# Kernel optimization log

Measured on AMD Instinct MI355X. Metric: run time of the kernel, lower is better.

## Reference

```python
import jax, jax.numpy as jnp
import numpy as np

B, S, E, H = 4, 2048, 512, 8
D = E // H


def setup_inputs() -> dict:
    key = jax.random.key(0)
    ks = jax.random.split(key, 12)
    sc = 0.02
    return {
        "x": jax.random.normal(ks[0], (B, S, E), jnp.float32),
        "edge_bias": jax.random.normal(ks[1], (B, S, S), jnp.float32),
        "attn_mask": jax.random.randint(ks[2], (B, 1, S, S), 0, 2, jnp.int32),
        "Wq": jax.random.normal(ks[3], (E, E), jnp.float32) * sc,
        "bq": jnp.zeros((E,), jnp.float32),
        "Wk": jax.random.normal(ks[4], (E, E), jnp.float32) * sc,
        "bk": jnp.zeros((E,), jnp.float32),
        "Wv": jax.random.normal(ks[5], (E, E), jnp.float32) * sc,
        "bv": jnp.zeros((E,), jnp.float32),
        "Wo": jax.random.normal(ks[6], (E, E), jnp.float32) * sc,
        "bo": jnp.zeros((E,), jnp.float32),
    }


def reference(x, edge_bias, attn_mask, Wq, bq, Wk, bk, Wv, bv, Wo, bo):
    scale = D ** -0.5
    # projections -> [B, H, S, D]
    def proj(W, b):
        return (x @ W.T + b).reshape(B, S, H, D).transpose(0, 2, 1, 3)
    q = proj(Wq, bq)
    k = proj(Wk, bk)
    v = proj(Wv, bv)
    # scores [B, H, S, S] with edge bias and mask before softmax
    scores = jnp.einsum("bhqd,bhkd->bhqk", q, k) * scale
    scores = scores + edge_bias[:, None, :, :]
    scores = jnp.where(attn_mask == 0, -jnp.inf, scores)
    probs = jax.nn.softmax(scores, axis=-1)
    out = jnp.einsum("bhqk,bhkd->bhqd", probs, v)
    out = out.transpose(0, 2, 1, 3).reshape(B, S, E)
    return out @ Wo.T + bo
```

## Files before the change

kernel.cpp:

```cpp
#include <hip/hip_runtime.h>
#include <hip/hip_bf16.h>
#include <stdint.h>

#define DEV static __device__ __forceinline__

typedef float f32x4 __attribute__((ext_vector_type(4)));
typedef int   i32x4 __attribute__((ext_vector_type(4)));
typedef unsigned short u16x4 __attribute__((ext_vector_type(4)));
typedef __bf16 bf16x8 __attribute__((ext_vector_type(8)));

constexpr int Bb = 4, Ss = 2048, Ee = 512, Hh = 8, Dd = 64;
constexpr float LOG2E = 1.4426950408889634f;

DEV unsigned short f2bf(float f) {
  unsigned u = __float_as_uint(f);
  u += 0x7fff + ((u >> 16) & 1);
  return (unsigned short)(u >> 16);
}
DEV float bf2f(unsigned short h) { return __uint_as_float(((unsigned)h) << 16); }

DEV void gload16(const void* g, void* l) {
  __builtin_amdgcn_global_load_lds((__attribute__((address_space(1))) void*)(g),
                                   (__attribute__((address_space(3))) void*)(l), 16, 0, 0);
}

__global__ void k_cvt(const float* __restrict__ src, unsigned short* __restrict__ dst, int n4) {
  int i = blockIdx.x * 256 + threadIdx.x;
  if (i >= n4) return;
  f32x4 v = *(const f32x4*)(src + (size_t)i * 4);
  u16x4 o;
#pragma unroll
  for (int j = 0; j < 4; ++j) o[j] = f2bf(v[j]);
  *(u16x4*)(dst + (size_t)i * 4) = o;
}

__global__ void k_mb(const float* __restrict__ bias, const int* __restrict__ mask,
                     unsigned short* __restrict__ mb, int n4) {
  int i = blockIdx.x * 256 + threadIdx.x;
  if (i >= n4) return;
  f32x4 v = *(const f32x4*)(bias + (size_t)i * 4);
  i32x4 m = *(const i32x4*)(mask + (size_t)i * 4);
  u16x4 o;
  const unsigned short NEG = f2bf(-1e38f * LOG2E);
#pragma unroll
  for (int j = 0; j < 4; ++j) o[j] = m[j] ? f2bf(v[j] * LOG2E) : NEG;
  *(u16x4*)(mb + (size_t)i * 4) = o;
}

template <int MODE>
__global__ __launch_bounds__(256) void k_gemm(
    const unsigned short* __restrict__ A, const unsigned short* __restrict__ Bw,
    const float* __restrict__ b0, const float* __restrict__ b1, const float* __restrict__ b2,
    unsigned short* __restrict__ oq, unsigned short* __restrict__ ok,
    unsigned short* __restrict__ ovt, float* __restrict__ of32) {
  __shared__ unsigned short Asl[128 * 32];
  __shared__ unsigned short Bsl[128 * 32];
  const int tid = threadIdx.x;
  const int wave = tid >> 6, lane = tid & 63;
  const int l15 = lane & 15, lg = lane >> 4;
  const int brow = blockIdx.x, bcol = blockIdx.y;
  const int wm = (wave >> 1) * 64, wn = (wave & 1) * 64;

  f32x4 acc[4][4] = {};

  for (int k0 = 0; k0 < 512; k0 += 32) {
    __syncthreads();
#pragma unroll
    for (int rnd = 0; rnd < 2; ++rnd) {
      int vid = rnd * 256 + tid;
      int r = vid >> 2, c = vid & 3;
      gload16(A + (size_t)(brow * 128 + r) * 512 + k0 + c * 8,
              Asl + (size_t)(rnd * 256 + wave * 64) * 8);
      gload16(Bw + (size_t)(bcol * 128 + r) * 512 + k0 + c * 8,
              Bsl + (size_t)(rnd * 256 + wave * 64) * 8);
    }
    __syncthreads();
    bf16x8 af[4], bfr[4];
#pragma unroll
    for (int m = 0; m < 4; ++m) af[m] = *(const bf16x8*)(Asl + (wm + m * 16 + l15) * 32 + lg * 8);
#pragma unroll
    for (int n = 0; n < 4; ++n) bfr[n] = *(const bf16x8*)(Bsl + (wn + n * 16 + l15) * 32 + lg * 8);
#pragma unroll
    for (int m = 0; m < 4; ++m)
#pragma unroll
      for (int n = 0; n < 4; ++n)
        acc[m][n] = __builtin_amdgcn_mfma_f32_16x16x32_bf16(af[m], bfr[n], acc[m][n], 0, 0, 0);
  }

  if (MODE == 0) {
    const int Nbase = bcol * 128;
    const int mat = Nbase >> 9;
    const int colb = Nbase & 511;
    const float* bp = (mat == 0) ? b0 : ((mat == 1) ? b1 : b2);
#pragma unroll
    for (int m = 0; m < 4; ++m)
#pragma unroll
      for (int n = 0; n < 4; ++n) {
        const int col = colb + wn + n * 16 + l15;
        const int h = col >> 6, d = col & 63;
        const float bv = bp[col];
#pragma unroll
        for (int j = 0; j < 4; ++j) {
          const int M = brow * 128 + wm + m * 16 + lg * 4 + j;
          const int b = M >> 11, s = M & 2047;
          float outv = acc[m][n][j] + bv;
          if (mat == 0) outv *= 0.125f * LOG2E;
          const unsigned short hv = f2bf(outv);
          if (mat == 0)
            oq[(((size_t)(b * Hh + h)) * Ss + s) * Dd + d] = hv;
          else if (mat == 1)
            ok[(((size_t)(b * Hh + h)) * Ss + s) * Dd + d] = hv;
          else
            ovt[(((size_t)(b * Hh + h)) * Dd + d) * Ss + s] = hv;
        }
      }
  } else {
#pragma unroll
    for (int m = 0; m < 4; ++m)
#pragma unroll
      for (int n = 0; n < 4; ++n) {
        const int col = bcol * 128 + wn + n * 16 + l15;
        const float bv = b0[col];
#pragma unroll
        for (int j = 0; j < 4; ++j) {
          const int M = brow * 128 + wm + m * 16 + lg * 4 + j;
          of32[(size_t)M * 512 + col] = acc[m][n][j] + bv;
        }
      }
  }
}

__global__ __launch_bounds__(256, 4) void k_attn(
    const unsigned short* __restrict__ q, const unsigned short* __restrict__ k,
    const unsigned short* __restrict__ vt, const unsigned short* __restrict__ mb,
    unsigned short* __restrict__ att) {
  __shared__ unsigned short Ksl[2][4096];
  __shared__ unsigned short Vsl[2][4096];
  __shared__ unsigned short Psl[4][1024];
  const int tid = threadIdx.x;
  const int wave = tid >> 6, lane = tid & 63;
  const int l15 = lane & 15, lg = lane >> 4;
  const int qt = blockIdx.x, bh = blockIdx.y;
  const int b = bh >> 3, h = bh & 7;
  const size_t qkb = (size_t)bh * Ss * Dd;
  const size_t vtbase = (size_t)bh * Dd * Ss;
  const int q0 = qt * 64 + wave * 16;
  const int qrow = q0 + l15;
  const int swz = (l15 & 7) << 3;

  bf16x8 qf[2];
#pragma unroll
  for (int ks = 0; ks < 2; ++ks)
    qf[ks] = *(const bf16x8*)(q + qkb + (size_t)qrow * Dd + ks * 32 + lg * 8);

  const size_t mbrow = ((size_t)b * Ss + qrow) * Ss;

  f32x4 accO[4] = {};
  float mrow = -INFINITY, lrow = 0.f;

  auto stage = [&](int buf, int t) {
    const int key0 = t * 64;
#pragma unroll
    for (int rnd = 0; rnd < 2; ++rnd) {
      int v2 = rnd * 256 + tid;
      int ks = v2 >> 8, r = (v2 >> 2) & 63, c = v2 & 3;
      gload16(k + qkb + (size_t)(key0 + r) * Dd + ks * 32 + c * 8,
              &Ksl[buf][(rnd * 256 + wave * 64) * 8]);
    }
#pragma unroll
    for (int rnd = 0; rnd < 2; ++rnd) {
      int v2 = rnd * 256 + tid;
      int ks = v2 >> 8, r = (v2 >> 2) & 63, c = v2 & 3;
      gload16(vt + vtbase + (size_t)r * Ss + key0 + ks * 32 + c * 8,
              &Vsl[buf][(rnd * 256 + wave * 64) * 8]);
    }
  };

  stage(0, 0);
  u16x4 bvc[4], bvn[4];
#pragma unroll
  for (int m = 0; m < 4; ++m) bvc[m] = *(const u16x4*)(mb + mbrow + m * 16 + lg * 4);

  for (int t = 0; t < 32; ++t) {
    const int cur = t & 1;
    __syncthreads();

    if (t < 31) {
      stage(cur ^ 1, t + 1);
#pragma unroll
      for (int m = 0; m < 4; ++m)
        bvn[m] = *(const u16x4*)(mb + mbrow + (t + 1) * 64 + m * 16 + lg * 4);
    }

    f32x4 sc[4] = {};
#pragma unroll
    for (int ks = 0; ks < 2; ++ks) {
      bf16x8 kfm[4];
#pragma unroll
      for (int m = 0; m < 4; ++m)
        kfm[m] = *(const bf16x8*)(&Ksl[cur][ks * 2048 + (m * 16 + l15) * 32 + lg * 8]);
#pragma unroll
      for (int m = 0; m < 4; ++m)
        sc[m] = __builtin_amdgcn_mfma_f32_16x16x32_bf16(kfm[m], qf[ks], sc[m], 0, 0, 0);
    }

    float pm = -INFINITY;
#pragma unroll
    for (int m = 0; m < 4; ++m)
#pragma unroll
      for (int j = 0; j < 4; ++j) {
        sc[m][j] += bf2f(bvc[m][j]);
        pm = fmaxf(pm, sc[m][j]);
      }
    pm = fmaxf(pm, __shfl_xor(pm, 16));
    pm = fmaxf(pm, __shfl_xor(pm, 32));
    const float mnew = fmaxf(mrow, pm);
    const float c = exp2f(mrow - mnew);
    mrow = mnew;
    float rs = 0.f;
#pragma unroll
    for (int m = 0; m < 4; ++m)
#pragma unroll
      for (int j = 0; j < 4; ++j) {
        const float p = exp2f(sc[m][j] - mnew);
        sc[m][j] = p;
        rs += p;
      }
    rs += __shfl_xor(rs, 16);
    rs += __shfl_xor(rs, 32);
    lrow = lrow * c + rs;
#pragma unroll
    for (int n = 0; n < 4; ++n) accO[n] *= c;

#pragma unroll
    for (int m = 0; m < 4; ++m) {
      u16x4 o;
#pragma unroll
      for (int j = 0; j < 4; ++j) o[j] = f2bf(sc[m][j]);
      *(u16x4*)(&Psl[wave][(l15 * 64 + m * 16 + lg * 4) ^ swz]) = o;
    }
    asm volatile("" ::: "memory");

#pragma unroll
    for (int ks2 = 0; ks2 < 2; ++ks2) {
      bf16x8 pB = *(const bf16x8*)(&Psl[wave][(l15 * 64 + ks2 * 32 + lg * 8) ^ swz]);
      bf16x8 va[4];
#pragma unroll
      for (int n = 0; n < 4; ++n)
        va[n] = *(const bf16x8*)(&Vsl[cur][ks2 * 2048 + (n * 16 + l15) * 32 + lg * 8]);
#pragma unroll
      for (int n = 0; n < 4; ++n)
        accO[n] = __builtin_amdgcn_mfma_f32_16x16x32_bf16(va[n], pB, accO[n], 0, 0, 0);
    }

#pragma unroll
    for (int m = 0; m < 4; ++m) bvc[m] = bvn[m];
  }

  const float invl = 1.0f / lrow;
#pragma unroll
  for (int n = 0; n < 4; ++n) {
    u16x4 o;
#pragma unroll
    for (int j = 0; j < 4; ++j) o[j] = f2bf(accO[n][j] * invl);
    *(u16x4*)(att + ((size_t)b * Ss + qrow) * Ee + h * Dd + n * 16 + lg * 4) = o;
  }
}

extern "C" void kernel_launch(void* const* d_in, const int* in_sizes, int n_in,
                              void* d_out, int out_size, void* d_ws, size_t ws_size,
                              hipStream_t stream) {
  const float* x  = (const float*)d_in[0];
  const float* eb = (const float*)d_in[1];
  const int*   am = (const int*)d_in[2];
  const float* Wq = (const float*)d_in[3];
  const float* bq = (const float*)d_in[4];
  const float* Wk = (const float*)d_in[5];
  const float* bk = (const float*)d_in[6];
  const float* Wv = (const float*)d_in[7];
  const float* bv = (const float*)d_in[8];
  const float* Wo = (const float*)d_in[9];
  const float* bo = (const float*)d_in[10];
  float* out = (float*)d_out;

  unsigned short* xb   = (unsigned short*)d_ws;
  unsigned short* wqkv = xb + (size_t)8192 * 512;
  unsigned short* wo   = wqkv + (size_t)1536 * 512;
  unsigned short* qb   = wo + (size_t)512 * 512;
  unsigned short* kb   = qb + (size_t)Bb * Hh * Ss * Dd;
  unsigned short* vtb  = kb + (size_t)Bb * Hh * Ss * Dd;
  unsigned short* attb = vtb + (size_t)Bb * Hh * Ss * Dd;
  unsigned short* mbb  = attb + (size_t)8192 * 512;

  k_cvt<<<4096, 256, 0, stream>>>(x, xb, 8192 * 512 / 4);
  k_cvt<<<256, 256, 0, stream>>>(Wq, wqkv, 512 * 512 / 4);
  k_cvt<<<256, 256, 0, stream>>>(Wk, wqkv + (size_t)512 * 512, 512 * 512 / 4);
  k_cvt<<<256, 256, 0, stream>>>(Wv, wqkv + (size_t)1024 * 512, 512 * 512 / 4);
  k_cvt<<<256, 256, 0, stream>>>(Wo, wo, 512 * 512 / 4);
  k_mb<<<16384, 256, 0, stream>>>(eb, am, mbb, Bb * Ss * Ss / 4);

  dim3 blk(256);
  dim3 g1(64, 12);
  k_gemm<0><<<g1, blk, 0, stream>>>(xb, wqkv, bq, bk, bv, qb, kb, vtb, nullptr);
  dim3 g2(32, 32);
  k_attn<<<g2, blk, 0, stream>>>(qb, kb, vtb, mbb, attb);
  dim3 g3(64, 4);
  k_gemm<1><<<g3, blk, 0, stream>>>(attb, wo, bo, nullptr, nullptr, nullptr, nullptr, nullptr, out);
}
```

Baseline: 186.7 us.

## Replace LDS round-trip for P with ds_bpermute register shuffle and packed bf16 convert

The softmax probabilities are converted with the hardware packed bf16 instruction and redistributed into the MFMA B-operand layout using ds_bpermute cross-lane shuffles, replacing the write and read through a per-wave LDS buffer. The online-softmax rescale of the accumulator and row sum is skipped when no row's max increased, using a wave-wide vote. This removes LDS store/load traffic and frees shared memory, which may raise occupancy. In exchange it issues eight bpermutes per k-step plus selects, and the hardware convert may round differently from the manual RNE code.

After: 181.1 us. 3.0% less time.

```diff
diff --git a/kernel.cpp b/kernel.cpp
--- a/kernel.cpp
+++ b/kernel.cpp
@@ -7,6 +7,7 @@
 typedef float f32x4 __attribute__((ext_vector_type(4)));
 typedef int   i32x4 __attribute__((ext_vector_type(4)));
 typedef unsigned short u16x4 __attribute__((ext_vector_type(4)));
+typedef unsigned u32x4 __attribute__((ext_vector_type(4)));
 typedef __bf16 bf16x8 __attribute__((ext_vector_type(8)));
 
 constexpr int Bb = 4, Ss = 2048, Ee = 512, Hh = 8, Dd = 64;
@@ -18,6 +19,12 @@
   return (unsigned short)(u >> 16);
 }
 DEV float bf2f(unsigned short h) { return __uint_as_float(((unsigned)h) << 16); }
+
+DEV unsigned cvtpk(float lo, float hi) {
+  unsigned r;
+  asm("v_cvt_pk_bf16_f32 %0, %1, %2" : "=v"(r) : "v"(lo), "v"(hi));
+  return r;
+}
 
 DEV void gload16(const void* g, void* l) {
   __builtin_amdgcn_global_load_lds((__attribute__((address_space(1))) void*)(g),
@@ -136,7 +143,6 @@
     unsigned short* __restrict__ att) {
   __shared__ unsigned short Ksl[2][4096];
   __shared__ unsigned short Vsl[2][4096];
-  __shared__ unsigned short Psl[4][1024];
   const int tid = threadIdx.x;
   const int wave = tid >> 6, lane = tid & 63;
   const int l15 = lane & 15, lg = lane >> 4;
@@ -146,7 +152,10 @@
   const size_t vtbase = (size_t)bh * Dd * Ss;
   const int q0 = qt * 64 + wave * 16;
   const int qrow = q0 + l15;
-  const int swz = (l15 & 7) << 3;
+
+  const int addrA = (l15 + 32 * (lg & 1)) * 4;
+  const int addrB = addrA + 64;
+  const bool hi = (lg >> 1) != 0;
 
   bf16x8 qf[2];
 #pragma unroll
@@ -215,7 +224,12 @@
     pm = fmaxf(pm, __shfl_xor(pm, 16));
     pm = fmaxf(pm, __shfl_xor(pm, 32));
     const float mnew = fmaxf(mrow, pm);
-    const float c = exp2f(mrow - mnew);
+    if (!__all(pm <= mrow)) {
+      const float c = exp2f(mrow - mnew);
+      lrow *= c;
+#pragma unroll
+      for (int n = 0; n < 4; ++n) accO[n] *= c;
+    }
     mrow = mnew;
     float rs = 0.f;
 #pragma unroll
@@ -228,26 +242,36 @@
       }
     rs += __shfl_xor(rs, 16);
     rs += __shfl_xor(rs, 32);
-    lrow = lrow * c + rs;
-#pragma unroll
-    for (int n = 0; n < 4; ++n) accO[n] *= c;
-
+    lrow += rs;
+
+    unsigned pk[4][2];
 #pragma unroll
     for (int m = 0; m < 4; ++m) {
-      u16x4 o;
-#pragma unroll
-      for (int j = 0; j < 4; ++j) o[j] = f2bf(sc[m][j]);
-      *(u16x4*)(&Psl[wave][(l15 * 64 + m * 16 + lg * 4) ^ swz]) = o;
-    }
-    asm volatile("" ::: "memory");
+      pk[m][0] = cvtpk(sc[m][0], sc[m][1]);
+      pk[m][1] = cvtpk(sc[m][2], sc[m][3]);
+    }
 
 #pragma unroll
     for (int ks2 = 0; ks2 < 2; ++ks2) {
-      bf16x8 pB = *(const bf16x8*)(&Psl[wave][(l15 * 64 + ks2 * 32 + lg * 8) ^ swz]);
       bf16x8 va[4];
 #pragma unroll
       for (int n = 0; n < 4; ++n)
         va[n] = *(const bf16x8*)(&Vsl[cur][ks2 * 2048 + (n * 16 + l15) * 32 + lg * 8]);
+      const int mlo = 2 * ks2, mhi = 2 * ks2 + 1;
+      unsigned lo0 = __builtin_amdgcn_ds_bpermute(addrA, pk[mlo][0]);
+      unsigned hi0 = __builtin_amdgcn_ds_bpermute(addrA, pk[mhi][0]);
+      unsigned lo1 = __builtin_amdgcn_ds_bpermute(addrA, pk[mlo][1]);
+      unsigned hi1 = __builtin_amdgcn_ds_bpermute(addrA, pk[mhi][1]);
+      unsigned lo2 = __builtin_amdgcn_ds_bpermute(addrB, pk[mlo][0]);
+      unsigned hi2 = __builtin_amdgcn_ds_bpermute(addrB, pk[mhi][0]);
+      unsigned lo3 = __builtin_amdgcn_ds_bpermute(addrB, pk[mlo][1]);
+      unsigned hi3 = __builtin_amdgcn_ds_bpermute(addrB, pk[mhi][1]);
+      u32x4 wv;
+      wv[0] = hi ? hi0 : lo0;
+      wv[1] = hi ? hi1 : lo1;
+      wv[2] = hi ? hi2 : lo2;
+      wv[3] = hi ? hi3 : lo3;
+      const bf16x8 pB = __builtin_bit_cast(bf16x8, wv);
 #pragma unroll
       for (int n = 0; n < 4; ++n)
         accO[n] = __builtin_amdgcn_mfma_f32_16x16x32_bf16(va[n], pB, accO[n], 0, 0, 0);
```
